# Kernel optimization log

Hardware: AMD Instinct MI355X
Metric: run time of the kernel (lower is better)

The kernel has to match this reference:

```python
import jax, jax.numpy as jnp
import numpy as np

EMBED_DIM = 2048
HEAD_DIM = 128


def setup_inputs() -> dict:
    key = jax.random.key(0)
    ks = jax.random.split(key, 7)
    B, S = 4, 2048
    lim = 1.0 / np.sqrt(EMBED_DIM)
    hidden_state = jax.random.normal(ks[0], (B, S, EMBED_DIM), dtype=jnp.float32)
    # nn.Linear weights stored as [out, in]; we keep [in, out] for x @ W
    Wq = jax.random.uniform(ks[1], (EMBED_DIM, HEAD_DIM), minval=-lim, maxval=lim, dtype=jnp.float32)
    Wk = jax.random.uniform(ks[2], (EMBED_DIM, HEAD_DIM), minval=-lim, maxval=lim, dtype=jnp.float32)
    Wv = jax.random.uniform(ks[3], (EMBED_DIM, HEAD_DIM), minval=-lim, maxval=lim, dtype=jnp.float32)
    bq = jax.random.uniform(ks[4], (HEAD_DIM,), minval=-lim, maxval=lim, dtype=jnp.float32)
    bk = jax.random.uniform(ks[5], (HEAD_DIM,), minval=-lim, maxval=lim, dtype=jnp.float32)
    bv = jax.random.uniform(ks[6], (HEAD_DIM,), minval=-lim, maxval=lim, dtype=jnp.float32)
    return {"hidden_state": hidden_state, "Wq": Wq, "bq": bq, "Wk": Wk, "bk": bk, "Wv": Wv, "bv": bv}


def reference(hidden_state, Wq, bq, Wk, bk, Wv, bv):
    q = hidden_state @ Wq + bq  # [B,S,D]
    k = hidden_state @ Wk + bk
    v = hidden_state @ Wv + bv
    scale = 1.0 / jnp.sqrt(jnp.asarray(HEAD_DIM, dtype=q.dtype))
    scores = jnp.einsum("bqd,bkd->bqk", q, k) * scale  # [B,S,S]
    S = q.shape[1]
    causal = jnp.triu(jnp.ones((S, S), dtype=bool), k=1)
    scores = jnp.where(causal, jnp.asarray(-1e10, dtype=scores.dtype), scores)
    weights = jax.nn.softmax(scores, axis=-1)
    return jnp.einsum("bqk,bkd->bqd", weights, v)
```

## Files before the change

### kernel.cpp

```cpp
#include <hip/hip_runtime.h>
#include <hip/hip_bf16.h>

#define EMBED 2048
#define SEQ   2048
#define BATCH 4
#define HD    128
#define MROWS (BATCH * SEQ)
#define NTOT  (3 * HD)
#define SCALE 0.08838834764831845f
#define NBQ   (SEQ / 64)
#define NSPL  6
#define FIXM  4.0f

typedef __attribute__((ext_vector_type(8))) short bf16x8;
typedef __attribute__((ext_vector_type(4))) float f32x4;

__device__ __forceinline__ unsigned short f2bf_rne(float x) {
    union { float f; unsigned u; } c; c.f = x;
    unsigned r = c.u + 0x7fffu + ((c.u >> 16) & 1u);
    return (unsigned short)(r >> 16);
}

#define MFMA16(a, b, c) __builtin_amdgcn_mfma_f32_16x16x32_bf16((a), (b), (c), 0, 0, 0)

__device__ __forceinline__ void gload_lds16(const unsigned short* gp, unsigned short* lp) {
    __builtin_amdgcn_global_load_lds(
        (const __attribute__((address_space(1))) void*)gp,
        (__attribute__((address_space(3))) void*)lp, 16, 0, 0);
}

__global__ __launch_bounds__(256) void h_conv(
    const float* __restrict__ H, unsigned short* __restrict__ Hbf)
{
    const size_t i = ((size_t)blockIdx.x * 256 + threadIdx.x) * 8;
    const float4 f0 = *(const float4*)(H + i);
    const float4 f1 = *(const float4*)(H + i + 4);
    union { unsigned short s[8]; uint4 v; } u;
    u.s[0] = f2bf_rne(f0.x); u.s[1] = f2bf_rne(f0.y);
    u.s[2] = f2bf_rne(f0.z); u.s[3] = f2bf_rne(f0.w);
    u.s[4] = f2bf_rne(f1.x); u.s[5] = f2bf_rne(f1.y);
    u.s[6] = f2bf_rne(f1.z); u.s[7] = f2bf_rne(f1.w);
    *(uint4*)(Hbf + i) = u.v;
}

__global__ __launch_bounds__(256) void wt_conv(
    const float* __restrict__ Wq, const float* __restrict__ Wk,
    const float* __restrict__ Wv, unsigned short* __restrict__ WT)
{
    __shared__ float lds[64][129];
    const int tid = threadIdx.x;
    const int blk = blockIdx.x;
    const int mat = blk >> 5;
    const int k0  = (blk & 31) * 64;
    const float* src = (mat == 0) ? Wq : (mat == 1) ? Wk : Wv;

    const float4* s4 = (const float4*)(src + (size_t)k0 * HD);
    for (int i = tid; i < 2048; i += 256) {
        const float4 v = s4[i];
        const int k  = i >> 5;
        const int n4 = (i & 31) * 4;
        lds[k][n4 + 0] = v.x; lds[k][n4 + 1] = v.y;
        lds[k][n4 + 2] = v.z; lds[k][n4 + 3] = v.w;
    }
    __syncthreads();

    const int n  = tid >> 1;
    const int kc = (tid & 1) * 32;
    unsigned short* dst = WT + ((size_t)(mat * HD + n)) * EMBED + k0 + kc;
#pragma unroll
    for (int c = 0; c < 4; ++c) {
        union { unsigned short s[8]; uint4 v; } u;
#pragma unroll
        for (int i = 0; i < 8; ++i)
            u.s[i] = f2bf_rne(lds[kc + c * 8 + i][n]);
        ((uint4*)dst)[c] = u.v;
    }
}

__global__ __launch_bounds__(256, 2) void gemm_qkv(
    const unsigned short* __restrict__ Hbf, const unsigned short* __restrict__ WT,
    const float* __restrict__ bq, const float* __restrict__ bk,
    const float* __restrict__ bv,
    unsigned short* __restrict__ Qbf, unsigned short* __restrict__ Kbf,
    unsigned short* __restrict__ VT)
{
    __shared__ unsigned short Abuf[128 * 64];
    __shared__ unsigned short Bbuf[64 * 64];

    const int tid  = threadIdx.x;
    const int w    = tid >> 6;
    const int lane = tid & 63;
    const int l16  = lane & 15;
    const int quad = lane >> 4;

    const int bid   = blockIdx.x;
    const int xcd   = bid & 7;
    const int local = bid >> 3;
    const int n_blk = local % 6;
    const int m_grp = local / 6;
    const int m0 = (m_grp * 8 + xcd) * 128;
    const int n0 = n_blk * 64;

    const int lr   = lane >> 3;
    const int slot = lane & 7;
    const int gch  = slot ^ lr;
    const unsigned short* ag[4]; unsigned short* al[4];
#pragma unroll
    for (int t = 0; t < 4; ++t) {
        const int r = (w * 4 + t) * 8 + lr;
        ag[t] = Hbf + (size_t)(m0 + r) * EMBED + gch * 8;
        al[t] = Abuf + (w * 4 + t) * 512;
    }
    const unsigned short* bg[2]; unsigned short* bl[2];
#pragma unroll
    for (int t = 0; t < 2; ++t) {
        const int r = (w * 2 + t) * 8 + lr;
        bg[t] = WT + (size_t)(n0 + r) * EMBED + gch * 8;
        bl[t] = Bbuf + (w * 2 + t) * 512;
    }

    const int wm = (w >> 1) * 64;
    const int wn = (w & 1) * 32;
    const int xq = l16 & 7;

    f32x4 acc[4][2];
#pragma unroll
    for (int mt = 0; mt < 4; ++mt)
#pragma unroll
        for (int nt = 0; nt < 2; ++nt) {
            f32x4 z = {0.f, 0.f, 0.f, 0.f};
            acc[mt][nt] = z;
        }

    for (int kt = 0; kt < EMBED / 64; ++kt) {
        const int ko = kt * 64;
#pragma unroll
        for (int t = 0; t < 4; ++t) gload_lds16(ag[t] + ko, al[t]);
#pragma unroll
        for (int t = 0; t < 2; ++t) gload_lds16(bg[t] + ko, bl[t]);
        __syncthreads();

        bf16x8 aF[4][2], bF[2][2];
#pragma unroll
        for (int mt = 0; mt < 4; ++mt)
#pragma unroll
            for (int ks = 0; ks < 2; ++ks)
                aF[mt][ks] = *(const bf16x8*)(
                    Abuf + (wm + mt * 16 + l16) * 64 + (((ks * 4 + quad) ^ xq) * 8));
#pragma unroll
        for (int nt = 0; nt < 2; ++nt)
#pragma unroll
            for (int ks = 0; ks < 2; ++ks)
                bF[nt][ks] = *(const bf16x8*)(
                    Bbuf + (wn + nt * 16 + l16) * 64 + (((ks * 4 + quad) ^ xq) * 8));
#pragma unroll
        for (int ks = 0; ks < 2; ++ks)
#pragma unroll
            for (int mt = 0; mt < 4; ++mt)
#pragma unroll
                for (int nt = 0; nt < 2; ++nt)
                    acc[mt][nt] = MFMA16(aF[mt][ks], bF[nt][ks], acc[mt][nt]);
        __syncthreads();
    }

#pragma unroll
    for (int nt = 0; nt < 2; ++nt) {
        const int col = n0 + wn + nt * 16 + l16;
        const int sel = col >> 7;
        const int c   = col & (HD - 1);
        const float bias = (sel == 0 ? bq : (sel == 1 ? bk : bv))[c];
#pragma unroll
        for (int mt = 0; mt < 4; ++mt) {
#pragma unroll
            for (int r = 0; r < 4; ++r) {
                const int row = m0 + wm + mt * 16 + quad * 4 + r;
                const float v = acc[mt][nt][r] + bias;
                if (sel == 0) {
                    Qbf[(size_t)row * HD + c] = f2bf_rne(v * SCALE);
                } else if (sel == 1) {
                    Kbf[(size_t)row * HD + c] = f2bf_rne(v);
                } else {
                    const int b = row >> 11;
                    const int s = row & (SEQ - 1);
                    VT[((size_t)b * HD + c) * SEQ + s] = f2bf_rne(v);
                }
            }
        }
    }
}

__global__ __launch_bounds__(256, 3) void flash_attn(
    const unsigned short* __restrict__ Qbf,
    const unsigned short* __restrict__ Kbf,
    const unsigned short* __restrict__ VT,
    float* __restrict__ pO, float* __restrict__ pL)
{
    __shared__ unsigned short Kbuf[64 * 128];
    __shared__ unsigned short Vbuf[128 * 64];
    __shared__ unsigned short plds[4][16 * 72];

    const int tid  = threadIdx.x;
    const int w    = tid >> 6;
    const int lane = tid & 63;
    const int l16  = lane & 15;
    const int quad = lane >> 4;
    const int b    = blockIdx.y;
    const int qb    = NBQ - 1 - blockIdx.x / NSPL;
    const int split = blockIdx.x % NSPL;
    const int q0    = qb * 64;
    const int qw0   = q0 + w * 16;

    bf16x8 aq[4];
    const unsigned short* qrow = Qbf + ((size_t)b * SEQ + qw0 + l16) * HD + quad * 8;
#pragma unroll
    for (int kt = 0; kt < 4; ++kt)
        aq[kt] = *(const bf16x8*)(qrow + kt * 32);

    f32x4 o[8];
#pragma unroll
    for (int nt = 0; nt < 8; ++nt) {
        f32x4 z = {0.f, 0.f, 0.f, 0.f};
        o[nt] = z;
    }
    float l_run[4];
#pragma unroll
    for (int r = 0; r < 4; ++r) l_run[r] = 0.f;

    const int lr4 = lane >> 4, sl4 = lane & 15;
    const int lr8 = lane >> 3, sl8 = lane & 7;
    const unsigned short* kbase = Kbf + (size_t)b * SEQ * HD;
    const unsigned short* vbase = VT + (size_t)b * HD * SEQ;
    unsigned short* myp = &plds[w][0];

    for (int t = split; t <= qb; t += NSPL) {
        const int j0 = t * 64;

#pragma unroll
        for (int i = 0; i < 4; ++i) {
            const int jl = w * 16 + i * 4 + lr4;
            gload_lds16(kbase + (size_t)(j0 + jl) * HD + (sl4 ^ (i * 4 + lr4)) * 8,
                        Kbuf + (w * 16 + i * 4) * 128);
        }
#pragma unroll
        for (int i = 0; i < 4; ++i) {
            const int dr = w * 32 + i * 8 + lr8;
            gload_lds16(vbase + (size_t)dr * SEQ + j0 + (sl8 ^ lr8) * 8,
                        Vbuf + (w * 32 + i * 8) * 64);
        }
        __syncthreads();

        if (j0 <= qw0 + 15) {
            f32x4 s[4];
#pragma unroll
            for (int nt = 0; nt < 4; ++nt) {
                f32x4 z = {0.f, 0.f, 0.f, 0.f};
                s[nt] = z;
            }
#pragma unroll
            for (int kt = 0; kt < 4; ++kt) {
#pragma unroll
                for (int nt = 0; nt < 4; ++nt) {
                    const bf16x8 bk = *(const bf16x8*)(
                        Kbuf + (nt * 16 + l16) * 128 + (((kt * 4 + quad) ^ l16) * 8));
                    s[nt] = MFMA16(aq[kt], bk, s[nt]);
                }
            }

#pragma unroll
            for (int nt = 0; nt < 4; ++nt) {
                const int j = j0 + nt * 16 + l16;
#pragma unroll
                for (int r = 0; r < 4; ++r) {
                    const int q = qw0 + quad * 4 + r;
                    const float sv = (j > q) ? -1e30f : s[nt][r];
                    const float pv = __expf(sv - FIXM);
                    l_run[r] += pv;
                    myp[(quad * 4 + r) * 72 + nt * 16 + l16] = f2bf_rne(pv);
                }
            }
            asm volatile("s_waitcnt lgkmcnt(0)" ::: "memory");
            const bf16x8 pf0 = *(const bf16x8*)(myp + l16 * 72 + quad * 8);
            const bf16x8 pf1 = *(const bf16x8*)(myp + l16 * 72 + 32 + quad * 8);

#pragma unroll
            for (int nt = 0; nt < 8; ++nt) {
                const bf16x8 bv0 = *(const bf16x8*)(
                    Vbuf + (nt * 16 + l16) * 64 + ((quad ^ (l16 & 7)) * 8));
                o[nt] = MFMA16(pf0, bv0, o[nt]);
            }
#pragma unroll
            for (int nt = 0; nt < 8; ++nt) {
                const bf16x8 bv1 = *(const bf16x8*)(
                    Vbuf + (nt * 16 + l16) * 64 + (((4 + quad) ^ (l16 & 7)) * 8));
                o[nt] = MFMA16(pf1, bv1, o[nt]);
            }
        }
        __syncthreads();
    }

#pragma unroll
    for (int r = 0; r < 4; ++r) {
#pragma unroll
        for (int d = 1; d < 16; d <<= 1)
            l_run[r] += __shfl_xor(l_run[r], d);
    }
    const int part = (b * NBQ + qb) * NSPL + split;
    float* po = pO + (size_t)part * (64 * HD);
#pragma unroll
    for (int nt = 0; nt < 8; ++nt)
#pragma unroll
        for (int r = 0; r < 4; ++r)
            po[(w * 16 + quad * 4 + r) * HD + nt * 16 + l16] = o[nt][r];
    if (l16 == 0) {
#pragma unroll
        for (int r = 0; r < 4; ++r)
            pL[part * 64 + w * 16 + quad * 4 + r] = l_run[r];
    }
}

__global__ __launch_bounds__(256) void attn_merge(
    const float* __restrict__ pO, const float* __restrict__ pL,
    float* __restrict__ out)
{
    const int qb = blockIdx.x;
    const int b  = blockIdx.y;
    const int tid = threadIdx.x;
    const int r  = tid >> 2;
    const int d0 = (tid & 3) * 32;
    const int p0 = (b * NBQ + qb) * NSPL;

    float L = 0.f;
#pragma unroll
    for (int s = 0; s < NSPL; ++s) L += pL[(p0 + s) * 64 + r];
    const float invL = 1.0f / L;

    float* op = out + ((size_t)b * SEQ + qb * 64 + r) * HD + d0;
#pragma unroll
    for (int c = 0; c < 8; ++c) {
        float4 acc = {0.f, 0.f, 0.f, 0.f};
#pragma unroll
        for (int s = 0; s < NSPL; ++s) {
            const float4 v = *(const float4*)(
                pO + (size_t)(p0 + s) * (64 * HD) + r * HD + d0 + c * 4);
            acc.x += v.x; acc.y += v.y; acc.z += v.z; acc.w += v.w;
        }
        op[c * 4 + 0] = acc.x * invL;
        op[c * 4 + 1] = acc.y * invL;
        op[c * 4 + 2] = acc.z * invL;
        op[c * 4 + 3] = acc.w * invL;
    }
}

extern "C" void kernel_launch(void* const* d_in, const int* in_sizes, int n_in,
                              void* d_out, int out_size, void* d_ws, size_t ws_size,
                              hipStream_t stream)
{
    const float* h  = (const float*)d_in[0];
    const float* Wq = (const float*)d_in[1];
    const float* bq = (const float*)d_in[2];
    const float* Wk = (const float*)d_in[3];
    const float* bk = (const float*)d_in[4];
    const float* Wv = (const float*)d_in[5];
    const float* bv = (const float*)d_in[6];
    float* out = (float*)d_out;

    unsigned short* Hbf = (unsigned short*)d_ws;
    unsigned short* Qbf = Hbf + (size_t)MROWS * EMBED;
    unsigned short* Kbf = Qbf + (size_t)MROWS * HD;
    unsigned short* VT  = Kbf + (size_t)MROWS * HD;
    unsigned short* WT  = VT  + (size_t)MROWS * HD;
    float* pO  = (float*)d_ws;
    float* pL  = pO + (size_t)BATCH * NBQ * NSPL * 64 * HD;

    h_conv<<<(MROWS * EMBED) / (256 * 8), 256, 0, stream>>>(h, Hbf);
    wt_conv<<<96, 256, 0, stream>>>(Wq, Wk, Wv, WT);
    gemm_qkv<<<384, 256, 0, stream>>>(Hbf, WT, bq, bk, bv, Qbf, Kbf, VT);
    flash_attn<<<dim3(NBQ * NSPL, BATCH), 256, 0, stream>>>(Qbf, Kbf, VT, pO, pL);
    attn_merge<<<dim3(NBQ, BATCH), 256, 0, stream>>>(pO, pL, out);
}
```

Measured before the change: 173.3 us.

## Double-buffer QKV GEMM LDS tiles and halve M tile to 64

The QKV projection GEMM now uses 64x64 output tiles instead of 128x64 and launches 768 blocks instead of 384, giving more blocks for occupancy across CUs. The LDS tiles are double-buffered so the async global-to-LDS load of the next K slice is issued before the MFMAs on the current slice, which drops one barrier per iteration. In exchange, per-block operand reuse falls, so more of the B matrix is re-read from memory, and launch bounds now target 3 blocks per CU.

```diff
diff --git a/kernel.cpp b/kernel.cpp
--- a/kernel.cpp
+++ b/kernel.cpp
@@ -77,15 +77,15 @@
     }
 }
 
-__global__ __launch_bounds__(256, 2) void gemm_qkv(
+__global__ __launch_bounds__(256, 3) void gemm_qkv(
     const unsigned short* __restrict__ Hbf, const unsigned short* __restrict__ WT,
     const float* __restrict__ bq, const float* __restrict__ bk,
     const float* __restrict__ bv,
     unsigned short* __restrict__ Qbf, unsigned short* __restrict__ Kbf,
     unsigned short* __restrict__ VT)
 {
-    __shared__ unsigned short Abuf[128 * 64];
-    __shared__ unsigned short Bbuf[64 * 64];
+    __shared__ unsigned short Abuf[2][64 * 64];
+    __shared__ unsigned short Bbuf[2][64 * 64];
 
     const int tid  = threadIdx.x;
     const int w    = tid >> 6;
@@ -98,68 +98,74 @@
     const int local = bid >> 3;
     const int n_blk = local % 6;
     const int m_grp = local / 6;
-    const int m0 = (m_grp * 8 + xcd) * 128;
+    const int m0 = (m_grp * 8 + xcd) * 64;
     const int n0 = n_blk * 64;
 
     const int lr   = lane >> 3;
     const int slot = lane & 7;
     const int gch  = slot ^ lr;
-    const unsigned short* ag[4]; unsigned short* al[4];
-#pragma unroll
-    for (int t = 0; t < 4; ++t) {
-        const int r = (w * 4 + t) * 8 + lr;
-        ag[t] = Hbf + (size_t)(m0 + r) * EMBED + gch * 8;
-        al[t] = Abuf + (w * 4 + t) * 512;
-    }
-    const unsigned short* bg[2]; unsigned short* bl[2];
+    const unsigned short* ag[2]; const unsigned short* bg[2];
+    int soff[2];
 #pragma unroll
     for (int t = 0; t < 2; ++t) {
         const int r = (w * 2 + t) * 8 + lr;
+        ag[t] = Hbf + (size_t)(m0 + r) * EMBED + gch * 8;
         bg[t] = WT + (size_t)(n0 + r) * EMBED + gch * 8;
-        bl[t] = Bbuf + (w * 2 + t) * 512;
-    }
-
-    const int wm = (w >> 1) * 64;
+        soff[t] = (w * 2 + t) * 512;
+    }
+
+    const int wm = (w >> 1) * 32;
     const int wn = (w & 1) * 32;
     const int xq = l16 & 7;
 
-    f32x4 acc[4][2];
-#pragma unroll
-    for (int mt = 0; mt < 4; ++mt)
+    f32x4 acc[2][2];
+#pragma unroll
+    for (int mt = 0; mt < 2; ++mt)
 #pragma unroll
         for (int nt = 0; nt < 2; ++nt) {
             f32x4 z = {0.f, 0.f, 0.f, 0.f};
             acc[mt][nt] = z;
         }
 
+#pragma unroll
+    for (int t = 0; t < 2; ++t) {
+        gload_lds16(ag[t], &Abuf[0][soff[t]]);
+        gload_lds16(bg[t], &Bbuf[0][soff[t]]);
+    }
+    __syncthreads();
+
     for (int kt = 0; kt < EMBED / 64; ++kt) {
-        const int ko = kt * 64;
-#pragma unroll
-        for (int t = 0; t < 4; ++t) gload_lds16(ag[t] + ko, al[t]);
-#pragma unroll
-        for (int t = 0; t < 2; ++t) gload_lds16(bg[t] + ko, bl[t]);
-        __syncthreads();
-
-        bf16x8 aF[4][2], bF[2][2];
-#pragma unroll
-        for (int mt = 0; mt < 4; ++mt)
+        const int cur = kt & 1;
+        if (kt + 1 < EMBED / 64) {
+            const int ko = (kt + 1) * 64;
+#pragma unroll
+            for (int t = 0; t < 2; ++t) {
+                gload_lds16(ag[t] + ko, &Abuf[cur ^ 1][soff[t]]);
+                gload_lds16(bg[t] + ko, &Bbuf[cur ^ 1][soff[t]]);
+            }
+        }
+
+        bf16x8 aF[2][2], bF[2][2];
+#pragma unroll
+        for (int mt = 0; mt < 2; ++mt)
 #pragma unroll
             for (int ks = 0; ks < 2; ++ks)
                 aF[mt][ks] = *(const bf16x8*)(
-                    Abuf + (wm + mt * 16 + l16) * 64 + (((ks * 4 + quad) ^ xq) * 8));
+                    &Abuf[cur][0] + (wm + mt * 16 + l16) * 64 + (((ks * 4 + quad) ^ xq) * 8));
 #pragma unroll
         for (int nt = 0; nt < 2; ++nt)
 #pragma unroll
             for (int ks = 0; ks < 2; ++ks)
                 bF[nt][ks] = *(const bf16x8*)(
-                    Bbuf + (wn + nt * 16 + l16) * 64 + (((ks * 4 + quad) ^ xq) * 8));
+                    &Bbuf[cur][0] + (wn + nt * 16 + l16) * 64 + (((ks * 4 + quad) ^ xq) * 8));
 #pragma unroll
         for (int ks = 0; ks < 2; ++ks)
 #pragma unroll
-            for (int mt = 0; mt < 4; ++mt)
+            for (int mt = 0; mt < 2; ++mt)
 #pragma unroll
                 for (int nt = 0; nt < 2; ++nt)
                     acc[mt][nt] = MFMA16(aF[mt][ks], bF[nt][ks], acc[mt][nt]);
+
         __syncthreads();
     }
 
@@ -170,7 +176,7 @@
         const int c   = col & (HD - 1);
         const float bias = (sel == 0 ? bq : (sel == 1 ? bk : bv))[c];
 #pragma unroll
-        for (int mt = 0; mt < 4; ++mt) {
+        for (int mt = 0; mt < 2; ++mt) {
 #pragma unroll
             for (int r = 0; r < 4; ++r) {
                 const int row = m0 + wm + mt * 16 + quad * 4 + r;
@@ -374,7 +380,7 @@
 
     h_conv<<<(MROWS * EMBED) / (256 * 8), 256, 0, stream>>>(h, Hbf);
     wt_conv<<<96, 256, 0, stream>>>(Wq, Wk, Wv, WT);
-    gemm_qkv<<<384, 256, 0, stream>>>(Hbf, WT, bq, bk, bv, Qbf, Kbf, VT);
+    gemm_qkv<<<768, 256, 0, stream>>>(Hbf, WT, bq, bk, bv, Qbf, Kbf, VT);
     flash_attn<<<dim3(NBQ * NSPL, BATCH), 256, 0, stream>>>(Qbf, Kbf, VT, pO, pL);
     attn_merge<<<dim3(NBQ, BATCH), 256, 0, stream>>>(pO, pL, out);
 }
```

New measurement: 169.3 us. -2.3%, faster.
